# Kernel optimization log

Measured on AMD Instinct MI355X. Metric: run time of the kernel, lower is better.

The kernel has to match this reference:

```python
import jax, jax.numpy as jnp
import numpy as np

N = 50000      # nodes
E = 800000     # edges (before self-loops)
IN = 256       # in_dim
HID = 64       # hidden_dim per head
HEADS = 4
OUT = 256      # out_dim
NEG_SLOPE = 0.2


def setup_inputs() -> dict:
    key = jax.random.key(0)
    ks = jax.random.split(key, 12)
    s = 0.1
    return {
        "x": jax.random.normal(ks[0], (N, IN), jnp.float32),
        "edge_index": jax.random.randint(ks[1], (2, E), 0, N, dtype=jnp.int32),
        # layer 1: GATConv(IN, HID, heads=HEADS, concat=True)
        "W1": jax.random.normal(ks[2], (IN, HEADS * HID), jnp.float32) * s,
        "att_src1": jax.random.normal(ks[3], (HEADS, HID), jnp.float32) * s,
        "att_dst1": jax.random.normal(ks[4], (HEADS, HID), jnp.float32) * s,
        "b1": jnp.zeros((HEADS * HID,), jnp.float32),
        # layer 2: GATConv(HEADS*HID, OUT, heads=1, concat=False)
        "W2": jax.random.normal(ks[5], (HEADS * HID, OUT), jnp.float32) * s,
        "att_src2": jax.random.normal(ks[6], (1, OUT), jnp.float32) * s,
        "att_dst2": jax.random.normal(ks[7], (1, OUT), jnp.float32) * s,
        "b2": jnp.zeros((OUT,), jnp.float32),
    }


def _gat_layer(x, src, dst, W, a_src, a_dst, b, heads, concat):
    n = x.shape[0]
    h = (x @ W).reshape(n, heads, -1)                     # [N,H,F]
    al_s = jnp.einsum('nhf,hf->nh', h, a_src)             # [N,H]
    al_d = jnp.einsum('nhf,hf->nh', h, a_dst)
    e = jax.nn.leaky_relu(al_s[src] + al_d[dst], NEG_SLOPE)  # [E,H]
    # segment softmax over incoming edges of each dst node
    m = jax.lax.stop_gradient(jax.ops.segment_max(e, dst, num_segments=n))
    ex = jnp.exp(e - m[dst])
    denom = jax.ops.segment_sum(ex, dst, num_segments=n)
    alpha = ex / (denom[dst] + 1e-16)                     # [E,H]
    out = jax.ops.segment_sum(h[src] * alpha[:, :, None], dst, num_segments=n)  # [N,H,F]
    out = out.reshape(n, -1) if concat else out.mean(axis=1)
    return out + b


def reference(x, edge_index, W1, att_src1, att_dst1, b1, W2, att_src2, att_dst2, b2):
    n = x.shape[0]
    loop = jnp.arange(n, dtype=edge_index.dtype)
    ei = jnp.concatenate([edge_index, jnp.stack([loop, loop])], axis=1)  # add self loops
    src, dst = ei[0], ei[1]
    h = _gat_layer(x, src, dst, W1, att_src1, att_dst1, b1, HEADS, True)
    h = jax.nn.elu(h)
    out = _gat_layer(h, src, dst, W2, att_src2, att_dst2, b2, 1, False)
    return out
```

## Files before the change

kernel.cpp:

```cpp
#include <hip/hip_runtime.h>
#include <math.h>

#define IN_DIM 256
#define FDIM 256
#define HEADS 4
#define NEG 0.2f
#define MAXD 96

typedef __attribute__((ext_vector_type(8))) short bf16x8;
typedef __attribute__((ext_vector_type(8))) unsigned short u16x8;
typedef __attribute__((ext_vector_type(4))) float f32x4;

__device__ __forceinline__ float leaky(float x){ return x > 0.f ? x : NEG * x; }

__device__ __forceinline__ unsigned short f2bf(float f){
  unsigned int u = __float_as_uint(f);
  unsigned int r = u + 0x7fffu + ((u >> 16) & 1u);
  return (unsigned short)(r >> 16);
}
__device__ __forceinline__ float bf2f(unsigned short s){
  return __uint_as_float(((unsigned int)s) << 16);
}

__device__ __forceinline__ float4 bcast4(float4 v){
  return make_float4(__shfl(v.x,0,64), __shfl(v.y,0,64), __shfl(v.z,0,64), __shfl(v.w,0,64));
}
__device__ __forceinline__ float comp4(float4 v, int h){
  return h==0 ? v.x : h==1 ? v.y : h==2 ? v.z : v.w;
}

__device__ __forceinline__ void gld_lds16(const void* g, void* l){
  __builtin_amdgcn_global_load_lds((const __attribute__((address_space(1))) unsigned int*)g,
                                   (__attribute__((address_space(3))) unsigned int*)l, 16, 0, 0);
}

__global__ void k_hist(const int* __restrict__ dst, int* deg, int E){
  int e = blockIdx.x * blockDim.x + threadIdx.x;
  if (e < E) atomicAdd(&deg[dst[e]], 1);
}

__global__ void k_scanA(const int* __restrict__ deg, int* tmp, int* partials, int n){
  __shared__ int sm[256];
  int i = blockIdx.x * 256 + threadIdx.x;
  int v = (i < n) ? deg[i] + 1 : 0;
  sm[threadIdx.x] = v; __syncthreads();
  for (int off = 1; off < 256; off <<= 1){
    int x = (threadIdx.x >= off) ? sm[threadIdx.x - off] : 0;
    __syncthreads();
    sm[threadIdx.x] += x;
    __syncthreads();
  }
  if (i < n) tmp[i] = sm[threadIdx.x];
  if (threadIdx.x == 255) partials[blockIdx.x] = sm[255];
}

__global__ void k_scanB(int* partials, int nb){
  __shared__ int sm[1024];
  int t = threadIdx.x;
  int v = (t < nb) ? partials[t] : 0;
  sm[t] = v; __syncthreads();
  for (int off = 1; off < 1024; off <<= 1){
    int x = (t >= off) ? sm[t - off] : 0;
    __syncthreads();
    sm[t] += x;
    __syncthreads();
  }
  if (t < nb) partials[t] = sm[t] - v;
}

__global__ void k_scanC(const int* __restrict__ tmp, const int* __restrict__ deg,
                        const int* __restrict__ partials, int* rowptr, int n){
  int i = blockIdx.x * blockDim.x + threadIdx.x;
  if (i < n){
    int incl = tmp[i] + partials[i >> 8];
    rowptr[i] = incl - (deg[i] + 1);
    if (i == n - 1) rowptr[n] = incl;
  }
}

__global__ void k_fill(const int* __restrict__ src, const int* __restrict__ dst,
                       const int* __restrict__ rowptr, int* fill, int* col, int E, int n){
  int e = blockIdx.x * blockDim.x + threadIdx.x;
  if (e < E + n){
    int s, d;
    if (e < E){ s = src[e]; d = dst[e]; } else { s = d = e - E; }
    int pos = atomicAdd(&fill[d], 1);
    col[rowptr[d] + pos] = s;
  }
}

__global__ void k_castwt(const float* __restrict__ x, unsigned short* __restrict__ xb, int M, int castBlocks,
                         const float* __restrict__ W1, unsigned short* __restrict__ W1t,
                         const float* __restrict__ W2, unsigned short* __restrict__ W2t){
  int b = blockIdx.x;
  if (b < castBlocks){
    int idx = b * 256 + threadIdx.x;
    int row = idx >> 6;
    float4 v = make_float4(0.f, 0.f, 0.f, 0.f);
    if (row < M) v = *(const float4*)(x + (size_t)idx * 4);
    ushort4 o;
    o.x = f2bf(v.x); o.y = f2bf(v.y); o.z = f2bf(v.z); o.w = f2bf(v.w);
    *(ushort4*)(xb + (size_t)idx * 4) = o;
  } else {
    int bb = b - castBlocks;
    const float* W = (bb < 256) ? W1 : W2;
    unsigned short* Wt = (bb < 256) ? W1t : W2t;
    int nn = bb & 255, k = threadIdx.x;
    Wt[nn * 256 + k] = f2bf(W[k * 256 + nn]);
  }
}

__global__ __launch_bounds__(256) void k_gemm(const unsigned short* __restrict__ A,
                                              const unsigned short* __restrict__ Bt,
                                              unsigned short* __restrict__ C,
                                              const float* __restrict__ asrc,
                                              const float* __restrict__ adst,
                                              float* __restrict__ als,
                                              float* __restrict__ ald,
                                              int nRows, int multi){
  __shared__ __align__(16) unsigned short sh[8192];
  unsigned short* As = sh;
  unsigned short* Bs = sh + 4096;
  int tid = threadIdx.x;
  int lane = tid & 63, wave = tid >> 6;
  int rowBase = blockIdx.x * 128, colBase = blockIdx.y * 128;
  int wr = (wave & 1) * 64, wc = (wave >> 1) * 64;

  f32x4 acc[4][4] = {};
  int c0 = tid, c1 = tid + 256;
  int r0 = c0 >> 2, kc0 = (c0 & 3) * 8;
  int r1 = c1 >> 2, kc1 = (c1 & 3) * 8;
  int m0 = lane & 15, kq = (lane >> 4) * 8;

  for (int k0 = 0; k0 < 256; k0 += 32){
    gld_lds16(A  + (size_t)(rowBase + r0) * 256 + k0 + kc0, (char*)As + c0 * 16);
    gld_lds16(A  + (size_t)(rowBase + r1) * 256 + k0 + kc1, (char*)As + c1 * 16);
    gld_lds16(Bt + (size_t)(colBase + r0) * 256 + k0 + kc0, (char*)Bs + c0 * 16);
    gld_lds16(Bt + (size_t)(colBase + r1) * 256 + k0 + kc1, (char*)Bs + c1 * 16);
    __syncthreads();
    bf16x8 af[4], bfr[4];
    #pragma unroll
    for (int it = 0; it < 4; ++it)
      af[it] = *(const bf16x8*)(As + (wr + it * 16 + m0) * 32 + kq);
    #pragma unroll
    for (int jt = 0; jt < 4; ++jt)
      bfr[jt] = *(const bf16x8*)(Bs + (wc + jt * 16 + m0) * 32 + kq);
    #pragma unroll
    for (int it = 0; it < 4; ++it)
      #pragma unroll
      for (int jt = 0; jt < 4; ++jt)
        acc[it][jt] = __builtin_amdgcn_mfma_f32_16x16x32_bf16(af[it], bfr[jt], acc[it][jt], 0, 0, 0);
    __syncthreads();
  }
  int cq = lane >> 4, cm = lane & 15;
  int sg = tid & 7;
  float accS[4] = {0.f,0.f,0.f,0.f}, accD[4] = {0.f,0.f,0.f,0.f};
  #pragma unroll
  for (int p = 0; p < 2; ++p){
    if ((wave >> 1) == p){
      #pragma unroll
      for (int it = 0; it < 4; ++it)
        #pragma unroll
        for (int jt = 0; jt < 4; ++jt)
          #pragma unroll
          for (int r = 0; r < 4; ++r)
            sh[(wr + it * 16 + cq * 4 + r) * 64 + jt * 16 + cm] = f2bf(acc[it][jt][r]);
    }
    __syncthreads();
    const float* asl = asrc + colBase + p * 64 + sg * 8;
    const float* adl = adst + colBase + p * 64 + sg * 8;
    float as8[8], ad8[8];
    #pragma unroll
    for (int k = 0; k < 8; ++k){ as8[k] = asl[k]; ad8[k] = adl[k]; }
    #pragma unroll
    for (int q = 0; q < 4; ++q){
      int id = tid + q * 256;
      int r = id >> 3;
      u16x8 v = *(const u16x8*)(sh + r * 64 + sg * 8);
      *(u16x8*)(C + (size_t)(rowBase + r) * 256 + colBase + p * 64 + sg * 8) = v;
      float ps = 0.f, pd = 0.f;
      #pragma unroll
      for (int k = 0; k < 8; ++k){
        float hv = bf2f((unsigned short)v[k]);
        ps += hv * as8[k]; pd += hv * ad8[k];
      }
      if (multi){
        #pragma unroll
        for (int off = 4; off >= 1; off >>= 1){
          ps += __shfl_down(ps, off, 8);
          pd += __shfl_down(pd, off, 8);
        }
        if (sg == 0){
          int grow = rowBase + r;
          if (grow < nRows){
            int hp = (colBase >> 6) + p;
            als[(size_t)grow * 4 + hp] = ps;
            ald[(size_t)grow * 4 + hp] = pd;
          }
        }
      } else {
        accS[q] += ps; accD[q] += pd;
      }
    }
    __syncthreads();
  }
  if (!multi){
    #pragma unroll
    for (int q = 0; q < 4; ++q){
      float ps = accS[q], pd = accD[q];
      #pragma unroll
      for (int off = 4; off >= 1; off >>= 1){
        ps += __shfl_down(ps, off, 8);
        pd += __shfl_down(pd, off, 8);
      }
      if (sg == 0){
        int r = (tid + q * 256) >> 3;
        int grow = rowBase + r;
        if (grow < nRows){
          atomicAdd(&als[grow], ps);
          atomicAdd(&ald[grow], pd);
        }
      }
    }
  }
}

__global__ __launch_bounds__(256) void k_agg1(const unsigned short* __restrict__ Hb,
    const float* __restrict__ als, const float* __restrict__ ald,
    const int* __restrict__ rowptr, const int* __restrict__ col,
    const float* __restrict__ b, unsigned short* __restrict__ outb, int n){
  __shared__ __align__(16) int   colS[4][MAXD];
  __shared__ __align__(16) float wS[4][MAXD][4];
  int wave = threadIdx.x >> 6, t = threadIdx.x & 63;
  int i = blockIdx.x * 4 + wave; if (i >= n) i = n - 1;
  int start = rowptr[i];
  int deg = rowptr[i + 1] - start;
  float4 adv = *(const float4*)(ald + (size_t)i * 4);
  bool staged = (deg <= MAXD);

  float4 ls = make_float4(0.f, 0.f, 0.f, 0.f);
  if (staged){
    for (int j = t; j < deg; j += 64){
      int s = col[start + j];
      colS[wave][j] = s;
      float4 a = *(const float4*)(als + (size_t)s * 4);
      float4 w = make_float4(__expf(leaky(a.x + adv.x)), __expf(leaky(a.y + adv.y)),
                             __expf(leaky(a.z + adv.z)), __expf(leaky(a.w + adv.w)));
      *(float4*)(&wS[wave][j][0]) = w;
      ls.x += w.x; ls.y += w.y; ls.z += w.z; ls.w += w.w;
    }
  } else {
    for (int j = t; j < deg; j += 64){
      int s = col[start + j];
      float4 a = *(const float4*)(als + (size_t)s * 4);
      ls.x += __expf(leaky(a.x + adv.x)); ls.y += __expf(leaky(a.y + adv.y));
      ls.z += __expf(leaky(a.z + adv.z)); ls.w += __expf(leaky(a.w + adv.w));
    }
  }
  #pragma unroll
  for (int off = 32; off >= 1; off >>= 1) ls = make_float4(
      ls.x + __shfl_down(ls.x, off, 64), ls.y + __shfl_down(ls.y, off, 64),
      ls.z + __shfl_down(ls.z, off, 64), ls.w + __shfl_down(ls.w, off, 64));
  float4 d4 = bcast4(ls);
  __syncthreads();

  int e2 = t >> 5, l32 = t & 31;
  int h = l32 >> 3, f = l32 * 8;
  float inv = 1.f / (comp4(d4, h) + 1e-16f);
  const unsigned short* Hrow = Hb + f;
  float a0[8] = {0,0,0,0,0,0,0,0}, a1[8] = {0,0,0,0,0,0,0,0};
  if (staged){
    int j = 0;
    for (; j + 3 < deg; j += 4){
      int j0 = j + e2, j1 = j + 2 + e2;
      int s0 = colS[wave][j0], s1 = colS[wave][j1];
      float w0 = wS[wave][j0][h], w1 = wS[wave][j1][h];
      u16x8 h0 = *(const u16x8*)(Hrow + (size_t)s0 * FDIM);
      u16x8 h1 = *(const u16x8*)(Hrow + (size_t)s1 * FDIM);
      #pragma unroll
      for (int k = 0; k < 8; ++k){ a0[k] += bf2f(h0[k]) * w0; a1[k] += bf2f(h1[k]) * w1; }
    }
    for (; j < deg; j += 2){
      int jj = j + e2;
      if (jj < deg){
        int s = colS[wave][jj]; float w = wS[wave][jj][h];
        u16x8 hh = *(const u16x8*)(Hrow + (size_t)s * FDIM);
        #pragma unroll
        for (int k = 0; k < 8; ++k) a0[k] += bf2f(hh[k]) * w;
      }
    }
  } else {
    float adh = comp4(adv, h);
    for (int j = e2; j < deg; j += 2){
      int s = col[start + j];
      float w = __expf(leaky(als[(size_t)s * 4 + h] + adh));
      u16x8 hh = *(const u16x8*)(Hrow + (size_t)s * FDIM);
      #pragma unroll
      for (int k = 0; k < 8; ++k) a0[k] += bf2f(hh[k]) * w;
    }
  }
  float r[8];
  #pragma unroll
  for (int k = 0; k < 8; ++k){
    r[k] = a0[k] + a1[k];
    r[k] += __shfl_down(r[k], 32, 64);
  }
  if (t < 32){
    float4 bA = *(const float4*)(b + f);
    float4 bB = *(const float4*)(b + f + 4);
    float bb[8] = {bA.x, bA.y, bA.z, bA.w, bB.x, bB.y, bB.z, bB.w};
    u16x8 o;
    #pragma unroll
    for (int k = 0; k < 8; ++k){
      float v = r[k] * inv + bb[k];
      v = (v > 0.f) ? v : (__expf(v) - 1.f);
      o[k] = f2bf(v);
    }
    *(u16x8*)(outb + (size_t)i * FDIM + f) = o;
  }
}

__global__ __launch_bounds__(256) void k_agg2(const unsigned short* __restrict__ Hb,
    const float* __restrict__ als, const float* __restrict__ ald,
    const int* __restrict__ rowptr, const int* __restrict__ col,
    const float* __restrict__ b, float* __restrict__ out, int n){
  __shared__ __align__(16) int   colS[4][MAXD];
  __shared__ __align__(16) float wS[4][MAXD];
  int wave = threadIdx.x >> 6, t = threadIdx.x & 63;
  int i = blockIdx.x * 4 + wave; if (i >= n) i = n - 1;
  int start = rowptr[i];
  int deg = rowptr[i + 1] - start;
  float adv = ald[i];
  bool staged = (deg <= MAXD);

  float ls = 0.f;
  if (staged){
    for (int j = t; j < deg; j += 64){
      int s = col[start + j];
      colS[wave][j] = s;
      float w = __expf(leaky(als[s] + adv));
      wS[wave][j] = w;
      ls += w;
    }
  } else {
    for (int j = t; j < deg; j += 64) ls += __expf(leaky(als[col[start + j]] + adv));
  }
  #pragma unroll
  for (int off = 32; off >= 1; off >>= 1) ls += __shfl_down(ls, off, 64);
  float inv = 1.f / (__shfl(ls, 0, 64) + 1e-16f);
  __syncthreads();

  int e2 = t >> 5, l32 = t & 31;
  int f = l32 * 8;
  const unsigned short* Hrow = Hb + f;
  float a0[8] = {0,0,0,0,0,0,0,0}, a1[8] = {0,0,0,0,0,0,0,0};
  if (staged){
    int j = 0;
    for (; j + 3 < deg; j += 4){
      int j0 = j + e2, j1 = j + 2 + e2;
      int s0 = colS[wave][j0], s1 = colS[wave][j1];
      float w0 = wS[wave][j0], w1 = wS[wave][j1];
      u16x8 h0 = *(const u16x8*)(Hrow + (size_t)s0 * FDIM);
      u16x8 h1 = *(const u16x8*)(Hrow + (size_t)s1 * FDIM);
      #pragma unroll
      for (int k = 0; k < 8; ++k){ a0[k] += bf2f(h0[k]) * w0; a1[k] += bf2f(h1[k]) * w1; }
    }
    for (; j < deg; j += 2){
      int jj = j + e2;
      if (jj < deg){
        int s = colS[wave][jj]; float w = wS[wave][jj];
        u16x8 hh = *(const u16x8*)(Hrow + (size_t)s * FDIM);
        #pragma unroll
        for (int k = 0; k < 8; ++k) a0[k] += bf2f(hh[k]) * w;
      }
    }
  } else {
    for (int j = e2; j < deg; j += 2){
      int s = col[start + j];
      float w = __expf(leaky(als[s] + adv));
      u16x8 hh = *(const u16x8*)(Hrow + (size_t)s * FDIM);
      #pragma unroll
      for (int k = 0; k < 8; ++k) a0[k] += bf2f(hh[k]) * w;
    }
  }
  float r[8];
  #pragma unroll
  for (int k = 0; k < 8; ++k){
    r[k] = a0[k] + a1[k];
    r[k] += __shfl_down(r[k], 32, 64);
  }
  if (t < 32){
    float4 bA = *(const float4*)(b + f);
    float4 bB = *(const float4*)(b + f + 4);
    float4 oA = make_float4(r[0]*inv + bA.x, r[1]*inv + bA.y, r[2]*inv + bA.z, r[3]*inv + bA.w);
    float4 oB = make_float4(r[4]*inv + bB.x, r[5]*inv + bB.y, r[6]*inv + bB.z, r[7]*inv + bB.w);
    *(float4*)(out + (size_t)i * FDIM + f) = oA;
    *(float4*)(out + (size_t)i * FDIM + f + 4) = oB;
  }
}

extern "C" void kernel_launch(void* const* d_in, const int* in_sizes, int n_in,
                              void* d_out, int out_size, void* d_ws, size_t ws_size,
                              hipStream_t stream){
  const float* x   = (const float*)d_in[0];
  const int*   ei  = (const int*)d_in[1];
  const float* W1  = (const float*)d_in[2];
  const float* as1 = (const float*)d_in[3];
  const float* ad1 = (const float*)d_in[4];
  const float* b1  = (const float*)d_in[5];
  const float* W2  = (const float*)d_in[6];
  const float* as2 = (const float*)d_in[7];
  const float* ad2 = (const float*)d_in[8];
  const float* b2  = (const float*)d_in[9];
  float* out = (float*)d_out;

  int n = in_sizes[0] / IN_DIM;
  int E = in_sizes[1] / 2;
  int Mpad = (n + 127) & ~127;
  const int* srcIdx = ei;
  const int* dstIdx = ei + E;

  char* ws = (char*)d_ws;
  size_t off = 0;
  auto alloc = [&](size_t bytes) -> void* {
    void* p = ws + off; off += (bytes + 255) & ~(size_t)255; return p;
  };
  unsigned short* bufA = (unsigned short*)alloc((size_t)Mpad * FDIM * 2);
  unsigned short* bufB = (unsigned short*)alloc((size_t)Mpad * FDIM * 2);
  unsigned short* W1t  = (unsigned short*)alloc(256 * 256 * 2);
  unsigned short* W2t  = (unsigned short*)alloc(256 * 256 * 2);
  int*   tmp      = (int*)alloc((size_t)n * 4);
  int*   deg      = (int*)alloc((size_t)n * 4);
  int*   fill     = (int*)alloc((size_t)n * 4);
  int*   rowptr   = (int*)alloc((size_t)(n + 1) * 4);
  int*   partials = (int*)alloc(1024 * 4);
  int*   col      = (int*)alloc((size_t)(E + n) * 4);
  float* als1     = (float*)alloc((size_t)n * HEADS * 4);
  float* ald1     = (float*)alloc((size_t)n * HEADS * 4);
  float* als2     = (float*)alloc((size_t)n * 4);
  float* ald2     = (float*)alloc((size_t)n * 4);
  (void)ws_size;

  int nb = (n + 255) / 256;
  hipMemsetAsync(deg, 0, (size_t)n * 4, stream);
  hipMemsetAsync(fill, 0, (size_t)n * 4, stream);
  hipMemsetAsync(als2, 0, (size_t)n * 4, stream);
  hipMemsetAsync(ald2, 0, (size_t)n * 4, stream);
  k_hist<<<(E + 255) / 256, 256, 0, stream>>>(dstIdx, deg, E);
  k_scanA<<<nb, 256, 0, stream>>>(deg, tmp, partials, n);
  k_scanB<<<1, 1024, 0, stream>>>(partials, nb);
  k_scanC<<<nb, 256, 0, stream>>>(tmp, deg, partials, rowptr, n);
  k_fill<<<(E + n + 255) / 256, 256, 0, stream>>>(srcIdx, dstIdx, rowptr, fill, col, E, n);

  int castBlocks = (Mpad * (FDIM / 4) + 255) / 256;
  k_castwt<<<castBlocks + 512, 256, 0, stream>>>(x, bufA, n, castBlocks, W1, W1t, W2, W2t);

  dim3 gg(Mpad / 128, FDIM / 128);
  int ga = (n + 3) / 4;
  k_gemm<<<gg, 256, 0, stream>>>(bufA, W1t, bufB, as1, ad1, als1, ald1, n, 1);
  k_agg1<<<ga, 256, 0, stream>>>(bufB, als1, ald1, rowptr, col, b1, bufA, n);
  k_gemm<<<gg, 256, 0, stream>>>(bufA, W2t, bufB, as2, ad2, als2, ald2, n, 0);
  k_agg2<<<ga, 256, 0, stream>>>(bufB, als2, ald2, rowptr, col, b2, out, n);
}
```

Measured before the change: 408.7 us.

## Restructure launch schedule: merge histogram, drop scan pass, split attention logits out of GEMM

Folds the degree histogram into the cast/transpose kernel and merges the two degree-array memsets into one. It also removes the single-block partials scan by having each scanC block sum its preceding partials with wave reductions. The attention logit dot products move out of the GEMM epilogue into separate lightweight kernels, which removes the atomic-based layer-2 path and its memsets. The aggregation kernels are split into two half-range launches. This cuts launch count and epilogue work in the GEMM, at the cost of an extra pass over H to compute the logits and extra launches for the split aggregation.

```diff
diff --git a/kernel.cpp b/kernel.cpp
--- a/kernel.cpp
+++ b/kernel.cpp
@@ -34,64 +34,10 @@
                                    (__attribute__((address_space(3))) unsigned int*)l, 16, 0, 0);
 }
 
-__global__ void k_hist(const int* __restrict__ dst, int* deg, int E){
-  int e = blockIdx.x * blockDim.x + threadIdx.x;
-  if (e < E) atomicAdd(&deg[dst[e]], 1);
-}
-
-__global__ void k_scanA(const int* __restrict__ deg, int* tmp, int* partials, int n){
-  __shared__ int sm[256];
-  int i = blockIdx.x * 256 + threadIdx.x;
-  int v = (i < n) ? deg[i] + 1 : 0;
-  sm[threadIdx.x] = v; __syncthreads();
-  for (int off = 1; off < 256; off <<= 1){
-    int x = (threadIdx.x >= off) ? sm[threadIdx.x - off] : 0;
-    __syncthreads();
-    sm[threadIdx.x] += x;
-    __syncthreads();
-  }
-  if (i < n) tmp[i] = sm[threadIdx.x];
-  if (threadIdx.x == 255) partials[blockIdx.x] = sm[255];
-}
-
-__global__ void k_scanB(int* partials, int nb){
-  __shared__ int sm[1024];
-  int t = threadIdx.x;
-  int v = (t < nb) ? partials[t] : 0;
-  sm[t] = v; __syncthreads();
-  for (int off = 1; off < 1024; off <<= 1){
-    int x = (t >= off) ? sm[t - off] : 0;
-    __syncthreads();
-    sm[t] += x;
-    __syncthreads();
-  }
-  if (t < nb) partials[t] = sm[t] - v;
-}
-
-__global__ void k_scanC(const int* __restrict__ tmp, const int* __restrict__ deg,
-                        const int* __restrict__ partials, int* rowptr, int n){
-  int i = blockIdx.x * blockDim.x + threadIdx.x;
-  if (i < n){
-    int incl = tmp[i] + partials[i >> 8];
-    rowptr[i] = incl - (deg[i] + 1);
-    if (i == n - 1) rowptr[n] = incl;
-  }
-}
-
-__global__ void k_fill(const int* __restrict__ src, const int* __restrict__ dst,
-                       const int* __restrict__ rowptr, int* fill, int* col, int E, int n){
-  int e = blockIdx.x * blockDim.x + threadIdx.x;
-  if (e < E + n){
-    int s, d;
-    if (e < E){ s = src[e]; d = dst[e]; } else { s = d = e - E; }
-    int pos = atomicAdd(&fill[d], 1);
-    col[rowptr[d] + pos] = s;
-  }
-}
-
 __global__ void k_castwt(const float* __restrict__ x, unsigned short* __restrict__ xb, int M, int castBlocks,
                          const float* __restrict__ W1, unsigned short* __restrict__ W1t,
-                         const float* __restrict__ W2, unsigned short* __restrict__ W2t){
+                         const float* __restrict__ W2, unsigned short* __restrict__ W2t,
+                         const int* __restrict__ dst, int* __restrict__ deg, int E){
   int b = blockIdx.x;
   if (b < castBlocks){
     int idx = b * 256 + threadIdx.x;
@@ -101,23 +47,66 @@
     ushort4 o;
     o.x = f2bf(v.x); o.y = f2bf(v.y); o.z = f2bf(v.z); o.w = f2bf(v.w);
     *(ushort4*)(xb + (size_t)idx * 4) = o;
-  } else {
+  } else if (b < castBlocks + 512){
     int bb = b - castBlocks;
     const float* W = (bb < 256) ? W1 : W2;
     unsigned short* Wt = (bb < 256) ? W1t : W2t;
     int nn = bb & 255, k = threadIdx.x;
     Wt[nn * 256 + k] = f2bf(W[k * 256 + nn]);
+  } else {
+    int e = (b - castBlocks - 512) * 256 + threadIdx.x;
+    if (e < E) atomicAdd(&deg[dst[e]], 1);
+  }
+}
+
+__global__ void k_scanA(const int* __restrict__ deg, int* tmp, int* partials, int n){
+  __shared__ int sm[256];
+  int i = blockIdx.x * 256 + threadIdx.x;
+  int v = (i < n) ? deg[i] + 1 : 0;
+  sm[threadIdx.x] = v; __syncthreads();
+  for (int off = 1; off < 256; off <<= 1){
+    int x = (threadIdx.x >= off) ? sm[threadIdx.x - off] : 0;
+    __syncthreads();
+    sm[threadIdx.x] += x;
+    __syncthreads();
+  }
+  if (i < n) tmp[i] = sm[threadIdx.x];
+  if (threadIdx.x == 255) partials[blockIdx.x] = sm[255];
+}
+
+__global__ void k_scanC(const int* __restrict__ tmp, const int* __restrict__ deg,
+                        const int* __restrict__ partials, int* rowptr, int n, int nb){
+  __shared__ int ws[4];
+  int bid = blockIdx.x, t = threadIdx.x;
+  int lane = t & 63, w = t >> 6;
+  int v = (t < bid && t < nb) ? partials[t] : 0;
+  #pragma unroll
+  for (int off = 32; off >= 1; off >>= 1) v += __shfl_down(v, off, 64);
+  if (lane == 0) ws[w] = v;
+  __syncthreads();
+  int prefix = ws[0] + ws[1] + ws[2] + ws[3];
+  int i = bid * 256 + t;
+  if (i < n){
+    int incl = tmp[i] + prefix;
+    rowptr[i] = incl - (deg[i] + 1);
+    if (i == n - 1) rowptr[n] = incl;
+  }
+}
+
+__global__ void k_fill(const int* __restrict__ src, const int* __restrict__ dst,
+                       const int* __restrict__ rowptr, int* fill, int* col, int E, int n){
+  int e = blockIdx.x * blockDim.x + threadIdx.x;
+  if (e < E + n){
+    int s, d;
+    if (e < E){ s = src[e]; d = dst[e]; } else { s = d = e - E; }
+    int pos = atomicAdd(&fill[d], 1);
+    col[rowptr[d] + pos] = s;
   }
 }
 
 __global__ __launch_bounds__(256) void k_gemm(const unsigned short* __restrict__ A,
                                               const unsigned short* __restrict__ Bt,
-                                              unsigned short* __restrict__ C,
-                                              const float* __restrict__ asrc,
-                                              const float* __restrict__ adst,
-                                              float* __restrict__ als,
-                                              float* __restrict__ ald,
-                                              int nRows, int multi){
+                                              unsigned short* __restrict__ C){
   __shared__ __align__(16) unsigned short sh[8192];
   unsigned short* As = sh;
   unsigned short* Bs = sh + 4096;
@@ -153,8 +142,6 @@
     __syncthreads();
   }
   int cq = lane >> 4, cm = lane & 15;
-  int sg = tid & 7;
-  float accS[4] = {0.f,0.f,0.f,0.f}, accD[4] = {0.f,0.f,0.f,0.f};
   #pragma unroll
   for (int p = 0; p < 2; ++p){
     if ((wave >> 1) == p){
@@ -167,72 +154,68 @@
             sh[(wr + it * 16 + cq * 4 + r) * 64 + jt * 16 + cm] = f2bf(acc[it][jt][r]);
     }
     __syncthreads();
-    const float* asl = asrc + colBase + p * 64 + sg * 8;
-    const float* adl = adst + colBase + p * 64 + sg * 8;
-    float as8[8], ad8[8];
-    #pragma unroll
-    for (int k = 0; k < 8; ++k){ as8[k] = asl[k]; ad8[k] = adl[k]; }
     #pragma unroll
     for (int q = 0; q < 4; ++q){
       int id = tid + q * 256;
-      int r = id >> 3;
+      int r = id >> 3, sg = id & 7;
       u16x8 v = *(const u16x8*)(sh + r * 64 + sg * 8);
       *(u16x8*)(C + (size_t)(rowBase + r) * 256 + colBase + p * 64 + sg * 8) = v;
-      float ps = 0.f, pd = 0.f;
-      #pragma unroll
-      for (int k = 0; k < 8; ++k){
-        float hv = bf2f((unsigned short)v[k]);
-        ps += hv * as8[k]; pd += hv * ad8[k];
-      }
-      if (multi){
-        #pragma unroll
-        for (int off = 4; off >= 1; off >>= 1){
-          ps += __shfl_down(ps, off, 8);
-          pd += __shfl_down(pd, off, 8);
-        }
-        if (sg == 0){
-          int grow = rowBase + r;
-          if (grow < nRows){
-            int hp = (colBase >> 6) + p;
-            als[(size_t)grow * 4 + hp] = ps;
-            ald[(size_t)grow * 4 + hp] = pd;
-          }
-        }
-      } else {
-        accS[q] += ps; accD[q] += pd;
-      }
-    }
-    __syncthreads();
-  }
-  if (!multi){
-    #pragma unroll
-    for (int q = 0; q < 4; ++q){
-      float ps = accS[q], pd = accD[q];
-      #pragma unroll
-      for (int off = 4; off >= 1; off >>= 1){
-        ps += __shfl_down(ps, off, 8);
-        pd += __shfl_down(pd, off, 8);
-      }
-      if (sg == 0){
-        int r = (tid + q * 256) >> 3;
-        int grow = rowBase + r;
-        if (grow < nRows){
-          atomicAdd(&als[grow], ps);
-          atomicAdd(&ald[grow], pd);
-        }
-      }
-    }
-  }
+    }
+    __syncthreads();
+  }
+}
+
+__global__ __launch_bounds__(256) void k_al4(const unsigned short* __restrict__ Hb,
+                      const float* __restrict__ as_, const float* __restrict__ ad_,
+                      float* als, float* ald, int n){
+  int wave = threadIdx.x >> 6, lane = threadIdx.x & 63;
+  int i = blockIdx.x * 4 + wave; if (i >= n) i = n - 1;
+  int f = lane * 4;
+  ushort4 hv = *(const ushort4*)(Hb + (size_t)i * FDIM + f);
+  float4 av = *(const float4*)(as_ + f);
+  float4 dv = *(const float4*)(ad_ + f);
+  float h0 = bf2f(hv.x), h1 = bf2f(hv.y), h2 = bf2f(hv.z), h3 = bf2f(hv.w);
+  float ps = h0*av.x + h1*av.y + h2*av.z + h3*av.w;
+  float pd = h0*dv.x + h1*dv.y + h2*dv.z + h3*dv.w;
+  #pragma unroll
+  for (int off = 8; off >= 1; off >>= 1){
+    ps += __shfl_down(ps, off, 16);
+    pd += __shfl_down(pd, off, 16);
+  }
+  if ((lane & 15) == 0){
+    int h = lane >> 4;
+    als[i * HEADS + h] = ps; ald[i * HEADS + h] = pd;
+  }
+}
+
+__global__ __launch_bounds__(256) void k_al1(const unsigned short* __restrict__ Hb,
+                      const float* __restrict__ as_, const float* __restrict__ ad_,
+                      float* als, float* ald, int n){
+  int wave = threadIdx.x >> 6, lane = threadIdx.x & 63;
+  int i = blockIdx.x * 4 + wave; if (i >= n) i = n - 1;
+  int f = lane * 4;
+  ushort4 hv = *(const ushort4*)(Hb + (size_t)i * FDIM + f);
+  float4 av = *(const float4*)(as_ + f);
+  float4 dv = *(const float4*)(ad_ + f);
+  float h0 = bf2f(hv.x), h1 = bf2f(hv.y), h2 = bf2f(hv.z), h3 = bf2f(hv.w);
+  float ps = h0*av.x + h1*av.y + h2*av.z + h3*av.w;
+  float pd = h0*dv.x + h1*dv.y + h2*dv.z + h3*dv.w;
+  #pragma unroll
+  for (int off = 32; off >= 1; off >>= 1){
+    ps += __shfl_down(ps, off, 64);
+    pd += __shfl_down(pd, off, 64);
+  }
+  if (lane == 0){ als[i] = ps; ald[i] = pd; }
 }
 
 __global__ __launch_bounds__(256) void k_agg1(const unsigned short* __restrict__ Hb,
     const float* __restrict__ als, const float* __restrict__ ald,
     const int* __restrict__ rowptr, const int* __restrict__ col,
-    const float* __restrict__ b, unsigned short* __restrict__ outb, int n){
+    const float* __restrict__ b, unsigned short* __restrict__ outb, int i0, int nEnd){
   __shared__ __align__(16) int   colS[4][MAXD];
   __shared__ __align__(16) float wS[4][MAXD][4];
   int wave = threadIdx.x >> 6, t = threadIdx.x & 63;
-  int i = blockIdx.x * 4 + wave; if (i >= n) i = n - 1;
+  int i = i0 + blockIdx.x * 4 + wave; if (i >= nEnd) i = nEnd - 1;
   int start = rowptr[i];
   int deg = rowptr[i + 1] - start;
   float4 adv = *(const float4*)(ald + (size_t)i * 4);
@@ -323,11 +306,11 @@
 __global__ __launch_bounds__(256) void k_agg2(const unsigned short* __restrict__ Hb,
     const float* __restrict__ als, const float* __restrict__ ald,
     const int* __restrict__ rowptr, const int* __restrict__ col,
-    const float* __restrict__ b, float* __restrict__ out, int n){
+    const float* __restrict__ b, float* __restrict__ out, int i0, int nEnd){
   __shared__ __align__(16) int   colS[4][MAXD];
   __shared__ __align__(16) float wS[4][MAXD];
   int wave = threadIdx.x >> 6, t = threadIdx.x & 63;
-  int i = blockIdx.x * 4 + wave; if (i >= n) i = n - 1;
+  int i = i0 + blockIdx.x * 4 + wave; if (i >= nEnd) i = nEnd - 1;
   int start = rowptr[i];
   int deg = rowptr[i + 1] - start;
   float adv = ald[i];
@@ -429,9 +412,10 @@
   unsigned short* bufB = (unsigned short*)alloc((size_t)Mpad * FDIM * 2);
   unsigned short* W1t  = (unsigned short*)alloc(256 * 256 * 2);
   unsigned short* W2t  = (unsigned short*)alloc(256 * 256 * 2);
+  int*   zeros    = (int*)alloc((size_t)n * 2 * 4);
+  int*   deg      = zeros;
+  int*   fill     = zeros + n;
   int*   tmp      = (int*)alloc((size_t)n * 4);
-  int*   deg      = (int*)alloc((size_t)n * 4);
-  int*   fill     = (int*)alloc((size_t)n * 4);
   int*   rowptr   = (int*)alloc((size_t)(n + 1) * 4);
   int*   partials = (int*)alloc(1024 * 4);
   int*   col      = (int*)alloc((size_t)(E + n) * 4);
@@ -442,23 +426,27 @@
   (void)ws_size;
 
   int nb = (n + 255) / 256;
-  hipMemsetAsync(deg, 0, (size_t)n * 4, stream);
-  hipMemsetAsync(fill, 0, (size_t)n * 4, stream);
-  hipMemsetAsync(als2, 0, (size_t)n * 4, stream);
-  hipMemsetAsync(ald2, 0, (size_t)n * 4, stream);
-  k_hist<<<(E + 255) / 256, 256, 0, stream>>>(dstIdx, deg, E);
+  hipMemsetAsync(zeros, 0, (size_t)n * 2 * 4, stream);
+
+  int castBlocks = (Mpad * (FDIM / 4) + 255) / 256;
+  int histBlocks = (E + 255) / 256;
+  k_castwt<<<castBlocks + 512 + histBlocks, 256, 0, stream>>>(
+      x, bufA, n, castBlocks, W1, W1t, W2, W2t, dstIdx, deg, E);
+
   k_scanA<<<nb, 256, 0, stream>>>(deg, tmp, partials, n);
-  k_scanB<<<1, 1024, 0, stream>>>(partials, nb);
-  k_scanC<<<nb, 256, 0, stream>>>(tmp, deg, partials, rowptr, n);
+  k_scanC<<<nb, 256, 0, stream>>>(tmp, deg, partials, rowptr, n, nb);
   k_fill<<<(E + n + 255) / 256, 256, 0, stream>>>(srcIdx, dstIdx, rowptr, fill, col, E, n);
-
-  int castBlocks = (Mpad * (FDIM / 4) + 255) / 256;
-  k_castwt<<<castBlocks + 512, 256, 0, stream>>>(x, bufA, n, castBlocks, W1, W1t, W2, W2t);
 
   dim3 gg(Mpad / 128, FDIM / 128);
   int ga = (n + 3) / 4;
-  k_gemm<<<gg, 256, 0, stream>>>(bufA, W1t, bufB, as1, ad1, als1, ald1, n, 1);
-  k_agg1<<<ga, 256, 0, stream>>>(bufB, als1, ald1, rowptr, col, b1, bufA, n);
-  k_gemm<<<gg, 256, 0, stream>>>(bufA, W2t, bufB, as2, ad2, als2, ald2, n, 0);
-  k_agg2<<<ga, 256, 0, stream>>>(bufB, als2, ald2, rowptr, col, b2, out, n);
-}
+  int nA = 25000;
+  int gaA = nA / 4, gaB = (n - nA + 3) / 4;
+  k_gemm<<<gg, 256, 0, stream>>>(bufA, W1t, bufB);
+  k_al4<<<ga, 256, 0, stream>>>(bufB, as1, ad1, als1, ald1, n);
+  k_agg1<<<gaA, 256, 0, stream>>>(bufB, als1, ald1, rowptr, col, b1, bufA, 0, nA);
+  k_agg1<<<gaB, 256, 0, stream>>>(bufB, als1, ald1, rowptr, col, b1, bufA, nA, n);
+  k_gemm<<<gg, 256, 0, stream>>>(bufA, W2t, bufB);
+  k_al1<<<ga, 256, 0, stream>>>(bufB, as2, ad2, als2, ald2, n);
+  k_agg2<<<gaA, 256, 0, stream>>>(bufB, als2, ald2, rowptr, col, b2, out, 0, nA);
+  k_agg2<<<gaB, 256, 0, stream>>>(bufB, als2, ald2, rowptr, col, b2, out, nA, n);
+}
```

Result: faster. 395.2 us (-3.3%).
